# Performance work log

Hardware: AMD Instinct MI355X
Metric: run time of the kernel (lower is better)

## Reference

```python
import jax, jax.numpy as jnp
import numpy as np
from jax import lax

N, T, H, E = 50000, 200, 128, 1600000


def setup_inputs() -> dict:
    key = jax.random.key(0)
    ks = jax.random.split(key, 32)
    s = 0.05
    inp = {}
    inp["lightcurve"] = jax.random.normal(ks[0], (N, T), dtype=jnp.float32)
    inp["edge_index"] = jax.random.randint(ks[1], (2, E), 0, N, dtype=jnp.int32)
    # LSTM layer 0 (input_dim=1) and layer 1 (input H), PyTorch gate order i,f,g,o
    inp["W_ih0"] = jax.random.normal(ks[2], (4 * H, 1), jnp.float32) * s
    inp["W_hh0"] = jax.random.normal(ks[3], (4 * H, H), jnp.float32) * s
    inp["b_ih0"] = jnp.zeros((4 * H,), jnp.float32)
    inp["b_hh0"] = jnp.zeros((4 * H,), jnp.float32)
    inp["W_ih1"] = jax.random.normal(ks[4], (4 * H, H), jnp.float32) * s
    inp["W_hh1"] = jax.random.normal(ks[5], (4 * H, H), jnp.float32) * s
    inp["b_ih1"] = jnp.zeros((4 * H,), jnp.float32)
    inp["b_hh1"] = jnp.zeros((4 * H,), jnp.float32)
    # 3 GCN conv layers + LayerNorms
    for i in range(3):
        inp[f"Wg{i}"] = jax.random.normal(ks[6 + i], (H, H), jnp.float32) * s
        inp[f"bg{i}"] = jnp.zeros((H,), jnp.float32)
        inp[f"gamma{i}"] = jnp.ones((H,), jnp.float32)
        inp[f"beta{i}"] = jnp.zeros((H,), jnp.float32)
    inp["W_out"] = jax.random.normal(ks[10], (H, 1), jnp.float32) * s
    inp["b_out"] = jnp.zeros((1,), jnp.float32)
    return inp


def _lstm_encode(x, W_ih0, W_hh0, b_ih0, b_hh0, W_ih1, W_hh1, b_ih1, b_hh1):
    # x: [N, T, 1] -> final hidden of layer 2: [N, H]. Both layers fused in one scan.
    n = x.shape[0]
    h = W_hh0.shape[1]

    def cell(xt, hs, cs, Wih, Whh, bih, bhh):
        g = xt @ Wih.T + hs @ Whh.T + (bih + bhh)
        i, f, gg, o = jnp.split(g, 4, axis=-1)
        cs = jax.nn.sigmoid(f) * cs + jax.nn.sigmoid(i) * jnp.tanh(gg)
        hs = jax.nn.sigmoid(o) * jnp.tanh(cs)
        return hs, cs

    def step(carry, x_t):
        h1, c1, h2, c2 = carry
        h1, c1 = cell(x_t, h1, c1, W_ih0, W_hh0, b_ih0, b_hh0)
        h2, c2 = cell(h1, h2, c2, W_ih1, W_hh1, b_ih1, b_hh1)
        return (h1, c1, h2, c2), None

    z = jnp.zeros((n, h), x.dtype)
    (_, _, h2, _), _ = lax.scan(step, (z, z, z, z), jnp.swapaxes(x, 0, 1))
    return h2


def _forward(lightcurve, W_ih0, W_hh0, b_ih0, b_hh0, W_ih1, W_hh1, b_ih1, b_hh1,
             Wg0, bg0, gamma0, beta0, Wg1, bg1, gamma1, beta1, Wg2, bg2, gamma2, beta2,
             W_out, b_out, edge_index):
    n = lightcurve.shape[0]
    h = _lstm_encode(lightcurve[..., None], W_ih0, W_hh0, b_ih0, b_hh0,
                     W_ih1, W_hh1, b_ih1, b_hh1)
    # GCN normalization (PyG GCNConv defaults: add self-loops, symmetric norm)
    loops = jnp.arange(n, dtype=edge_index.dtype)
    row = jnp.concatenate([edge_index[0], loops])  # source
    col = jnp.concatenate([edge_index[1], loops])  # target
    deg = jax.ops.segment_sum(jnp.ones_like(col, dtype=h.dtype), col, num_segments=n)
    dinv = lax.rsqrt(jnp.maximum(deg, 1.0))
    enorm = dinv[row] * dinv[col]  # [E+N]
    for Wg, bg, gm, bt in ((Wg0, bg0, gamma0, beta0), (Wg1, bg1, gamma1, beta1), (Wg2, bg2, gamma2, beta2)):
        h_prev = h
        msg = (h @ Wg)[row] * enorm[:, None]            # gather + scale
        h = jax.ops.segment_sum(msg, col, num_segments=n) + bg  # scatter-add
        mu = h.mean(-1, keepdims=True)                  # LayerNorm
        var = jnp.mean((h - mu) ** 2, axis=-1, keepdims=True)
        h = (h - mu) * lax.rsqrt(var + 1e-5) * gm + bt
        h = jax.nn.relu(h)
        h = h + h_prev  # dropout is identity in eval mode
    pooled = h.mean(axis=0, keepdims=True)  # [1, H]
    return pooled @ W_out + b_out           # [1, 1]


def reference(lightcurve, edge_index, W_ih0, W_hh0, b_ih0, b_hh0,
              W_ih1, W_hh1, b_ih1, b_hh1,
              Wg0, bg0, gamma0, beta0, Wg1, bg1, gamma1, beta1,
              Wg2, bg2, gamma2, beta2, W_out, b_out):
    return _forward(lightcurve, W_ih0, W_hh0, b_ih0, b_hh0, W_ih1, W_hh1, b_ih1, b_hh1,
                    Wg0, bg0, gamma0, beta0, Wg1, bg1, gamma1, beta1,
                    Wg2, bg2, gamma2, beta2, W_out, b_out, edge_index)
```

## Files before the change

### kernel.cpp

```cpp
#include <hip/hip_runtime.h>

#define NN 50000
#define TT 200
#define HH 128
#define EE 1600000

#define NL2E  -1.4426950408889634f
#define TWOL2E 2.8853900817779268f

typedef _Float16 f16x8 __attribute__((ext_vector_type(8)));
typedef float f32x4 __attribute__((ext_vector_type(4)));

__device__ __forceinline__ float sg2(float x) {
    return __builtin_amdgcn_rcpf(1.f + __builtin_amdgcn_exp2f(x));
}
__device__ __forceinline__ float th2(float x) {
    return 1.f - 2.f * __builtin_amdgcn_rcpf(__builtin_amdgcn_exp2f(x) + 1.f);
}
__device__ __forceinline__ f32x4 sg2_4(f32x4 x) {
    f32x4 r; r[0] = sg2(x[0]); r[1] = sg2(x[1]); r[2] = sg2(x[2]); r[3] = sg2(x[3]); return r;
}
__device__ __forceinline__ f32x4 th2_4(f32x4 x) {
    f32x4 r; r[0] = th2(x[0]); r[1] = th2(x[1]); r[2] = th2(x[2]); r[3] = th2(x[3]); return r;
}
__device__ __forceinline__ f32x4 splat4(float s) { f32x4 r = {s, s, s, s}; return r; }
__device__ __forceinline__ unsigned short f2h_bits(float x) {
    _Float16 h = (_Float16)x;
    union { _Float16 h; unsigned short u; } cv; cv.h = h; return cv.u;
}
__device__ __forceinline__ float h2f_bits(unsigned short u) {
    union { _Float16 h; unsigned short u; } cv; cv.u = u; return (float)cv.h;
}

__global__ void pack_w(const float* __restrict__ W, unsigned short* __restrict__ out) {
    int tile = blockIdx.x;
    int jn = tile >> 2, kk = tile & 3;
    int L = threadIdx.x;
    int n = jn * 16 + (L & 15);
    int k0 = kk * 32 + (L >> 4) * 8;
    float sc = ((jn >> 3) == 2) ? TWOL2E : NL2E;
    unsigned short* dst = out + (size_t)tile * 512 + L * 8;
#pragma unroll
    for (int i = 0; i < 8; ++i) dst[i] = f2h_bits(W[n * 128 + k0 + i] * sc);
}

__global__ void bias_prep(const float* __restrict__ bih0, const float* __restrict__ bhh0,
                          const float* __restrict__ bih1, const float* __restrict__ bhh1,
                          const float* __restrict__ wih0,
                          float* __restrict__ b0g, float* __restrict__ b1g, float* __restrict__ wxg) {
    int i = blockIdx.x * 256 + threadIdx.x;
    if (i < 512) {
        float sc = ((i >> 7) == 2) ? TWOL2E : NL2E;
        b0g[i] = (bih0[i] + bhh0[i]) * sc;
        b1g[i] = (bih1[i] + bhh1[i]) * sc;
        wxg[i] = wih0[i] * sc;
    }
}

__global__ void transpose_lc(const float* __restrict__ lc, float* __restrict__ xT) {
    __shared__ float tile[32][33];
    int tx = threadIdx.x, ty = threadIdx.y;
    int n0 = blockIdx.y * 32, t0 = blockIdx.x * 32;
#pragma unroll
    for (int i = 0; i < 32; i += 8) {
        int n = n0 + ty + i, t = t0 + tx;
        if (n < NN && t < TT) tile[ty + i][tx] = lc[(size_t)n * TT + t];
    }
    __syncthreads();
#pragma unroll
    for (int i = 0; i < 32; i += 8) {
        int t = t0 + ty + i, n = n0 + tx;
        if (n < NN && t < TT) xT[(size_t)t * NN + n] = tile[tx][ty + i];
    }
}


#define MFMA16(A, B, C) __builtin_amdgcn_mfma_f32_16x16x32_f16((A), (B), (C), 0, 0, 0)

#define MMC(HB, PI, PF, PG, PO, KK) {                                          \
    f16x8 bI_ = *reinterpret_cast<const f16x8*>((PI) + (KK) * 512);            \
    f16x8 bF_ = *reinterpret_cast<const f16x8*>((PF) + (KK) * 512);            \
    f16x8 bG_ = *reinterpret_cast<const f16x8*>((PG) + (KK) * 512);            \
    f16x8 bO_ = *reinterpret_cast<const f16x8*>((PO) + (KK) * 512);            \
    f16x8 a0_ = *reinterpret_cast<const f16x8*>(&(HB)[col][(KK) * 32 + quad * 8]);      \
    f16x8 a1_ = *reinterpret_cast<const f16x8*>(&(HB)[16 + col][(KK) * 32 + quad * 8]); \
    aI0 = MFMA16(a0_, bI_, aI0); aI1 = MFMA16(a1_, bI_, aI1);                  \
    aF0 = MFMA16(a0_, bF_, aF0); aF1 = MFMA16(a1_, bF_, aF1);                  \
    aG0 = MFMA16(a0_, bG_, aG0); aG1 = MFMA16(a1_, bG_, aG1);                  \
    aO0 = MFMA16(a0_, bO_, aO0); aO1 = MFMA16(a1_, bO_, aO1);                  \
}

#define ACT0N(RT, C, H, AI, AF, AG, AO) {                                      \
    f32x4 xv_ = *reinterpret_cast<const f32x4*>(&xs[(RT) * 16 + quad * 4]);    \
    f32x4 gi_ = AI + splat4(bI) + xv_ * splat4(wI);                            \
    f32x4 gf_ = AF + splat4(bF) + xv_ * splat4(wF);                            \
    f32x4 gg_ = AG + splat4(bG) + xv_ * splat4(wG);                            \
    f32x4 go_ = AO + splat4(bO) + xv_ * splat4(wO);                            \
    C = sg2_4(gf_) * C + sg2_4(gi_) * th2_4(gg_);                              \
    H = sg2_4(go_) * th2_4(C * splat4(TWOL2E));                                \
}

#define ACT1N(C, H, AI, AF, AG, AO) {                                          \
    f32x4 gi_ = AI + splat4(bI);                                               \
    f32x4 gf_ = AF + splat4(bF);                                               \
    f32x4 gg_ = AG + splat4(bG);                                               \
    f32x4 go_ = AO + splat4(bO);                                               \
    C = sg2_4(gf_) * C + sg2_4(gi_) * th2_4(gg_);                              \
    H = sg2_4(go_) * th2_4(C * splat4(TWOL2E));                                \
}

#define WRH(HB, RT, H)                                                         \
    (HB)[(RT) * 16 + quad * 4 + 0][j_] = f2h_bits((H)[0]);                     \
    (HB)[(RT) * 16 + quad * 4 + 1][j_] = f2h_bits((H)[1]);                     \
    (HB)[(RT) * 16 + quad * 4 + 2][j_] = f2h_bits((H)[2]);                     \
    (HB)[(RT) * 16 + quad * 4 + 3][j_] = f2h_bits((H)[3]);

#define STEP(PB, RB, T)                                                        \
    {                      \
        f32x4 aI0 = {}, aI1 = {}, aF0 = {}, aF1 = {};                          \
        f32x4 aG0 = {}, aG1 = {}, aO0 = {}, aO1 = {};                          \
        MMC(h1s[RB], p0I, p0F, p0G, p0O, 0)                                    \
        MMC(h1s[RB], p0I, p0F, p0G, p0O, 1)                                    \
        MMC(h1s[RB], p0I, p0F, p0G, p0O, 2)                                    \
        MMC(h1s[RB], p0I, p0F, p0G, p0O, 3)                                    \
        const float bI = b0s[j_], bF = b0s[128 + j_];                          \
        const float bG = b0s[256 + j_], bO = b0s[384 + j_];                    \
        const float wI = wxs[j_], wF = wxs[128 + j_];                          \
        const float wG = wxs[256 + j_], wO = wxs[384 + j_];                    \
        f32x4 h1v0, h1v1;                                                      \
        ACT0N(0, c1_0, h1v0, aI0, aF0, aG0, aO0)                               \
        ACT0N(1, c1_1, h1v1, aI1, aF1, aG1, aO1)                               \
        WRH(h1s[PB], 0, h1v0)                                                  \
        WRH(h1s[PB], 1, h1v1)                                                  \
    }                                                                          \
    __syncthreads();                                                           \
    {             \
        f32x4 aI0 = {}, aI1 = {}, aF0 = {}, aF1 = {};                          \
        f32x4 aG0 = {}, aG1 = {}, aO0 = {}, aO1 = {};                          \
        MMC(h1s[PB], u0I, u0F, u0G, u0O, 0)                                    \
        MMC(h1s[PB], u0I, u0F, u0G, u0O, 1)                                    \
        MMC(h1s[PB], u0I, u0F, u0G, u0O, 2)                                    \
        MMC(h1s[PB], u0I, u0F, u0G, u0O, 3)                                    \
        MMC(h2s[RB], v0I, v0F, v0G, v0O, 0)                                    \
        MMC(h2s[RB], v0I, v0F, v0G, v0O, 1)                                    \
        MMC(h2s[RB], v0I, v0F, v0G, v0O, 2)                                    \
        MMC(h2s[RB], v0I, v0F, v0G, v0O, 3)                                    \
        if (tid < 32) {                    \
            int n_ = n0 + tid;                                                 \
            xs[tid] = ((T) + 1 < TT && n_ < NN)                                \
                          ? xT[(size_t)((T) + 1) * NN + n_] : 0.f;             \
        }                                                                      \
        const float bI = b1s[j_], bF = b1s[128 + j_];                          \
        const float bG = b1s[256 + j_], bO = b1s[384 + j_];                    \
        f32x4 h2v0, h2v1;                                                      \
        ACT1N(c2_0, h2v0, aI0, aF0, aG0, aO0)                                  \
        ACT1N(c2_1, h2v1, aI1, aF1, aG1, aO1)                                  \
        WRH(h2s[PB], 0, h2v0)                                                  \
        WRH(h2s[PB], 1, h2v1)                                                  \
    }                                                                          \
    __syncthreads();

__global__ __launch_bounds__(512, 2) void lstm_kernel(
    const float* __restrict__ xT,
    const unsigned short* __restrict__ w0p,
    const unsigned short* __restrict__ w1ip,
    const unsigned short* __restrict__ w1hp,
    const float* __restrict__ b0g, const float* __restrict__ b1g,
    const float* __restrict__ wxg,
    float* __restrict__ h2out) {
    __shared__ unsigned short h1s[2][32][136];
    __shared__ unsigned short h2s[2][32][136];
    __shared__ __align__(16) float xs[32];
    __shared__ float b0s[512], b1s[512], wxs[512];

    const int tid = threadIdx.x;
    const int w = tid >> 6;
    const int lane = tid & 63;
    const int col = lane & 15;
    const int quad = lane >> 4;
    const int n0 = blockIdx.x * 32;
    const int j_ = w * 16 + col;

    for (int i = tid; i < 2 * 32 * 136; i += 512) {
        (&h1s[0][0][0])[i] = 0; (&h2s[0][0][0])[i] = 0;
    }
    if (tid < 512) { b0s[tid] = b0g[tid]; b1s[tid] = b1g[tid]; wxs[tid] = wxg[tid]; }
    if (tid < 32) { int n = n0 + tid; xs[tid] = (n < NN) ? xT[n] : 0.f; }

    const unsigned short* p0I = w0p + (size_t)w * 2048 + lane * 8;
    const unsigned short* p0F = w0p + (size_t)(8 + w) * 2048 + lane * 8;
    const unsigned short* p0G = w0p + (size_t)(16 + w) * 2048 + lane * 8;
    const unsigned short* p0O = w0p + (size_t)(24 + w) * 2048 + lane * 8;
    const unsigned short* u0I = w1ip + (size_t)w * 2048 + lane * 8;
    const unsigned short* u0F = w1ip + (size_t)(8 + w) * 2048 + lane * 8;
    const unsigned short* u0G = w1ip + (size_t)(16 + w) * 2048 + lane * 8;
    const unsigned short* u0O = w1ip + (size_t)(24 + w) * 2048 + lane * 8;
    const unsigned short* v0I = w1hp + (size_t)w * 2048 + lane * 8;
    const unsigned short* v0F = w1hp + (size_t)(8 + w) * 2048 + lane * 8;
    const unsigned short* v0G = w1hp + (size_t)(16 + w) * 2048 + lane * 8;
    const unsigned short* v0O = w1hp + (size_t)(24 + w) * 2048 + lane * 8;

    f32x4 c1_0 = {}, c1_1 = {}, c2_0 = {}, c2_1 = {};

    __syncthreads();

#pragma unroll 1
    for (int tt = 0; tt < TT; tt += 2) {
        STEP(0, 1, tt)
        STEP(1, 0, tt + 1)
    }

    for (int i = tid; i < 32 * 128; i += 512) {
        int m = i >> 7, j = i & 127;
        int n = n0 + m;
        if (n < NN) h2out[(size_t)n * HH + j] = h2f_bits(h2s[1][m][j]);
    }
}

__global__ void deg_init(float* __restrict__ deg) {
    int i = blockIdx.x * 256 + threadIdx.x;
    if (i < NN) deg[i] = 1.f;
}
__global__ void deg_edges(const int* __restrict__ ei, float* __restrict__ deg) {
    int e = blockIdx.x * 256 + threadIdx.x;
    if (e < EE) unsafeAtomicAdd(&deg[ei[EE + e]], 1.f);
}
__global__ void dinv_k(const float* __restrict__ deg, float* __restrict__ dinv) {
    int i = blockIdx.x * 256 + threadIdx.x;
    if (i < NN) dinv[i] = rsqrtf(fmaxf(deg[i], 1.f));
}

__global__ void scan_off(const float* __restrict__ deg, int* __restrict__ off) {
    __shared__ int sp[256];
    const int tid = threadIdx.x;
    const int chunk = (NN + 255) / 256;
    const int i0 = tid * chunk;
    int s = 0;
    for (int i = 0; i < chunk; ++i) {
        int idx = i0 + i;
        if (idx < NN) s += (int)deg[idx] - 1;
    }
    sp[tid] = s;
    __syncthreads();
    for (int o = 1; o < 256; o <<= 1) {
        int v = (tid >= o) ? sp[tid - o] : 0;
        __syncthreads();
        sp[tid] += v;
        __syncthreads();
    }
    int run = sp[tid] - s;
    for (int i = 0; i < chunk; ++i) {
        int idx = i0 + i;
        if (idx < NN) { off[idx] = run; run += (int)deg[idx] - 1; }
    }
    if (tid == 255) off[NN] = sp[255];
}

__global__ void csr_fill(const int* __restrict__ ei, const float* __restrict__ dinv,
                         const int* __restrict__ off, int* __restrict__ cur,
                         int* __restrict__ crow, float* __restrict__ cw) {
    int e = blockIdx.x * 256 + threadIdx.x;
    if (e >= EE) return;
    int r = ei[e], c = ei[EE + e];
    int p = atomicAdd(&cur[c], 1);
    int idx = off[c] + p;
    crow[idx] = r;
    cw[idx] = dinv[r] * dinv[c];
}

__global__ void gcn_gemm(const float* __restrict__ h, const float* __restrict__ Wg,
                         float* __restrict__ hw) {
    __shared__ float hsT[128][36];
    int tid = threadIdx.x;
    int n0 = blockIdx.x * 32;
#pragma unroll
    for (int c = 0; c < 16; ++c) {
        int lin = c * 256 + tid;
        int m = lin >> 7, k = lin & 127;
        int n = n0 + m;
        hsT[k][m] = (n < NN) ? h[(size_t)n * HH + k] : 0.f;
    }
    __syncthreads();
    int j = tid & 127, p = tid >> 7;
    float acc[16];
#pragma unroll
    for (int m = 0; m < 16; ++m) acc[m] = 0.f;
    for (int k = 0; k < 128; ++k) {
        float wg = Wg[k * 128 + j];
        const float4* hp = reinterpret_cast<const float4*>(&hsT[k][p * 16]);
        float4 a = hp[0], b = hp[1], c = hp[2], d = hp[3];
        acc[0]  += a.x * wg; acc[1]  += a.y * wg; acc[2]  += a.z * wg; acc[3]  += a.w * wg;
        acc[4]  += b.x * wg; acc[5]  += b.y * wg; acc[6]  += b.z * wg; acc[7]  += b.w * wg;
        acc[8]  += c.x * wg; acc[9]  += c.y * wg; acc[10] += c.z * wg; acc[11] += c.w * wg;
        acc[12] += d.x * wg; acc[13] += d.y * wg; acc[14] += d.z * wg; acc[15] += d.w * wg;
    }
#pragma unroll
    for (int m = 0; m < 16; ++m) {
        int n = n0 + p * 16 + m;
        if (n < NN) hw[(size_t)n * HH + j] = acc[m];
    }
}

__global__ __launch_bounds__(256) void gcn_agg(
    const float* __restrict__ hw, const int* __restrict__ off,
    const int* __restrict__ crow, const float* __restrict__ cw,
    const float* __restrict__ dinv, const float* __restrict__ bg,
    const float* __restrict__ gamma, const float* __restrict__ beta,
    float* __restrict__ h) {
    __shared__ float xch[4][2];
    const int tid = threadIdx.x;
    const int half = tid >> 7;
    const int f = tid & 127;
    const int v = blockIdx.x * 2 + half;
    const float d = dinv[v];
    float acc = bg[f] + d * d * hw[v * HH + f];
    const int s1 = off[v + 1];
    for (int s = off[v]; s < s1; ++s) {
        int r = crow[s];
        float wv = cw[s];
        acc = fmaf(wv, hw[r * HH + f], acc);
    }
    float sum = acc, sq = acc * acc;
#pragma unroll
    for (int o = 32; o; o >>= 1) { sum += __shfl_xor(sum, o); sq += __shfl_xor(sq, o); }
    int wid = tid >> 6;
    if ((tid & 63) == 0) { xch[wid][0] = sum; xch[wid][1] = sq; }
    __syncthreads();
    sum += xch[wid ^ 1][0]; sq += xch[wid ^ 1][1];
    float mu = sum * (1.f / 128.f);
    float var = sq * (1.f / 128.f) - mu * mu;
    float rn = rsqrtf(var + 1e-5f);
    float o = (acc - mu) * rn * gamma[f] + beta[f];
    h[v * HH + f] = fmaxf(o, 0.f) + h[v * HH + f];
}

__global__ void pool_k(const float* __restrict__ h, float* __restrict__ pooled) {
    int j = threadIdx.x & 127, p = threadIdx.x >> 7;
    float s = 0.f;
    for (int n = blockIdx.x * 2 + p; n < NN; n += 512) s += h[(size_t)n * HH + j];
    unsafeAtomicAdd(&pooled[j], s);
}

__global__ void final_k(const float* __restrict__ pooled, const float* __restrict__ Wout,
                        const float* __restrict__ bout, float* __restrict__ out) {
    int lane = threadIdx.x;
    float s = pooled[lane] * Wout[lane] + pooled[lane + 64] * Wout[lane + 64];
#pragma unroll
    for (int o = 32; o; o >>= 1) s += __shfl_xor(s, o);
    if (lane == 0) out[0] = s * (1.f / (float)NN) + bout[0];
}

extern "C" void kernel_launch(void* const* d_in, const int* in_sizes, int n_in,
                              void* d_out, int out_size, void* d_ws, size_t ws_size,
                              hipStream_t stream) {
    const float* lc   = (const float*)d_in[0];
    const int*   ei   = (const int*)d_in[1];
    const float* Wih0 = (const float*)d_in[2];
    const float* Whh0 = (const float*)d_in[3];
    const float* bih0 = (const float*)d_in[4];
    const float* bhh0 = (const float*)d_in[5];
    const float* Wih1 = (const float*)d_in[6];
    const float* Whh1 = (const float*)d_in[7];
    const float* bih1 = (const float*)d_in[8];
    const float* bhh1 = (const float*)d_in[9];
    const float* Wout = (const float*)d_in[22];
    const float* bout = (const float*)d_in[23];
    float* out = (float*)d_out;

    float* ws   = (float*)d_ws;
    float* h    = ws;
    float* hw   = ws + 6400000;
    float* xT   = ws + 6400000;
    int*   off  = (int*)(ws + 12800000);
    int*   cur  = off + 50048;
    int*   crow = cur + 50048;
    float* cw   = (float*)(crow + EE);
    float* P      = ws + 16400064;
    float* deg    = P;
    float* dinv   = deg + 50000;
    float* b0g    = dinv + 50000;
    float* b1g    = b0g + 512;
    float* wxg    = b1g + 512;
    float* pooled = wxg + 512;
    unsigned short* w0p  = (unsigned short*)(pooled + 128);
    unsigned short* w1ip = w0p + 65536;
    unsigned short* w1hp = w1ip + 65536;

    pack_w<<<128, 64, 0, stream>>>(Whh0, w0p);
    pack_w<<<128, 64, 0, stream>>>(Wih1, w1ip);
    pack_w<<<128, 64, 0, stream>>>(Whh1, w1hp);
    bias_prep<<<2, 256, 0, stream>>>(bih0, bhh0, bih1, bhh1, Wih0, b0g, b1g, wxg);
    {
        dim3 g((TT + 31) / 32, (NN + 31) / 32), b(32, 8);
        transpose_lc<<<g, b, 0, stream>>>(lc, xT);
    }
    deg_init<<<(NN + 255) / 256, 256, 0, stream>>>(deg);
    deg_edges<<<(EE + 255) / 256, 256, 0, stream>>>(ei, deg);
    dinv_k<<<(NN + 255) / 256, 256, 0, stream>>>(deg, dinv);

    lstm_kernel<<<(NN + 31) / 32, 512, 0, stream>>>(xT, w0p, w1ip, w1hp, b0g, b1g, wxg, h);

    hipMemsetAsync(cur, 0, 50000 * sizeof(int), stream);
    scan_off<<<1, 256, 0, stream>>>(deg, off);
    csr_fill<<<(EE + 255) / 256, 256, 0, stream>>>(ei, dinv, off, cur, crow, cw);

    for (int l = 0; l < 3; ++l) {
        const float* Wg = (const float*)d_in[10 + 4 * l];
        const float* bg = (const float*)d_in[11 + 4 * l];
        const float* gm = (const float*)d_in[12 + 4 * l];
        const float* bt = (const float*)d_in[13 + 4 * l];
        gcn_gemm<<<(NN + 31) / 32, 256, 0, stream>>>(h, Wg, hw);
        gcn_agg<<<NN / 2, 256, 0, stream>>>(hw, off, crow, cw, dinv, bg, gm, bt, h);
    }

    hipMemsetAsync(pooled, 0, HH * sizeof(float), stream);
    pool_k<<<256, 256, 0, stream>>>(h, pooled);
    final_k<<<1, 64, 0, stream>>>(pooled, Wout, bout, out);
}
```

Before: 7.786 ms.

## Halve LSTM block to 256 threads with each wave covering two hidden column groups

The LSTM kernel now launches 4 waves per block instead of 8. Each wave handles two 16-column hidden slices (j and j+64), so per-wave MFMA work doubles and the cell/hidden state registers double. Weight offsets become 32-bit indices into the packed matrices rather than twelve precomputed pointers. The aim is to cut the cost of block-wide barriers across fewer waves and to gain more instruction-level parallelism per wave. In exchange, register pressure rises and there are fewer waves available to hide latency.

Result: slower. 17.74 ms (+127.8%).

```diff
diff --git a/kernel.cpp b/kernel.cpp
--- a/kernel.cpp
+++ b/kernel.cpp
@@ -77,11 +77,14 @@
 
 #define MFMA16(A, B, C) __builtin_amdgcn_mfma_f32_16x16x32_f16((A), (B), (C), 0, 0, 0)
 
-#define MMC(HB, PI, PF, PG, PO, KK) {                                          \
-    f16x8 bI_ = *reinterpret_cast<const f16x8*>((PI) + (KK) * 512);            \
-    f16x8 bF_ = *reinterpret_cast<const f16x8*>((PF) + (KK) * 512);            \
-    f16x8 bG_ = *reinterpret_cast<const f16x8*>((PG) + (KK) * 512);            \
-    f16x8 bO_ = *reinterpret_cast<const f16x8*>((PO) + (KK) * 512);            \
+#define LD8(MAT, VO, KK) \
+    (*reinterpret_cast<const f16x8*>(&(MAT)[(size_t)(VO) + (KK) * 512]))
+
+#define MMCG(HB, MAT, VI, VF, VG, VOO, KK) {                                   \
+    f16x8 bI_ = LD8(MAT, VI, KK);                                              \
+    f16x8 bF_ = LD8(MAT, VF, KK);                                              \
+    f16x8 bG_ = LD8(MAT, VG, KK);                                              \
+    f16x8 bO_ = LD8(MAT, VOO, KK);                                             \
     f16x8 a0_ = *reinterpret_cast<const f16x8*>(&(HB)[col][(KK) * 32 + quad * 8]);      \
     f16x8 a1_ = *reinterpret_cast<const f16x8*>(&(HB)[16 + col][(KK) * 32 + quad * 8]); \
     aI0 = MFMA16(a0_, bI_, aI0); aI1 = MFMA16(a1_, bI_, aI1);                  \
@@ -109,58 +112,64 @@
     H = sg2_4(go_) * th2_4(C * splat4(TWOL2E));                                \
 }
 
-#define WRH(HB, RT, H)                                                         \
-    (HB)[(RT) * 16 + quad * 4 + 0][j_] = f2h_bits((H)[0]);                     \
-    (HB)[(RT) * 16 + quad * 4 + 1][j_] = f2h_bits((H)[1]);                     \
-    (HB)[(RT) * 16 + quad * 4 + 2][j_] = f2h_bits((H)[2]);                     \
-    (HB)[(RT) * 16 + quad * 4 + 3][j_] = f2h_bits((H)[3]);
+#define WRH(HB, RT, H, J)                                                      \
+    (HB)[(RT) * 16 + quad * 4 + 0][J] = f2h_bits((H)[0]);                      \
+    (HB)[(RT) * 16 + quad * 4 + 1][J] = f2h_bits((H)[1]);                      \
+    (HB)[(RT) * 16 + quad * 4 + 2][J] = f2h_bits((H)[2]);                      \
+    (HB)[(RT) * 16 + quad * 4 + 3][J] = f2h_bits((H)[3]);
+
+#define L0_GROUP(RB, PB, J, VI, VF, VG, VO_, C0, C1) {                         \
+    f32x4 aI0 = {}, aI1 = {}, aF0 = {}, aF1 = {};                              \
+    f32x4 aG0 = {}, aG1 = {}, aO0 = {}, aO1 = {};                              \
+    MMCG(h1s[RB], w0p, VI, VF, VG, VO_, 0)                                     \
+    MMCG(h1s[RB], w0p, VI, VF, VG, VO_, 1)                                     \
+    MMCG(h1s[RB], w0p, VI, VF, VG, VO_, 2)                                     \
+    MMCG(h1s[RB], w0p, VI, VF, VG, VO_, 3)                                     \
+    const float bI = b0s[J], bF = b0s[128 + (J)];                              \
+    const float bG = b0s[256 + (J)], bO = b0s[384 + (J)];                      \
+    const float wI = wxs[J], wF = wxs[128 + (J)];                              \
+    const float wG = wxs[256 + (J)], wO = wxs[384 + (J)];                      \
+    f32x4 h1v0, h1v1;                                                          \
+    ACT0N(0, C0, h1v0, aI0, aF0, aG0, aO0)                                     \
+    ACT0N(1, C1, h1v1, aI1, aF1, aG1, aO1)                                     \
+    WRH(h1s[PB], 0, h1v0, J)                                                   \
+    WRH(h1s[PB], 1, h1v1, J)                                                   \
+}
+
+#define L1_GROUP(RB, PB, J, VI, VF, VG, VO_, C0, C1) {                         \
+    f32x4 aI0 = {}, aI1 = {}, aF0 = {}, aF1 = {};                              \
+    f32x4 aG0 = {}, aG1 = {}, aO0 = {}, aO1 = {};                              \
+    MMCG(h1s[PB], w1ip, VI, VF, VG, VO_, 0)                                    \
+    MMCG(h1s[PB], w1ip, VI, VF, VG, VO_, 1)                                    \
+    MMCG(h1s[PB], w1ip, VI, VF, VG, VO_, 2)                                    \
+    MMCG(h1s[PB], w1ip, VI, VF, VG, VO_, 3)                                    \
+    MMCG(h2s[RB], w1hp, VI, VF, VG, VO_, 0)                                    \
+    MMCG(h2s[RB], w1hp, VI, VF, VG, VO_, 1)                                    \
+    MMCG(h2s[RB], w1hp, VI, VF, VG, VO_, 2)                                    \
+    MMCG(h2s[RB], w1hp, VI, VF, VG, VO_, 3)                                    \
+    const float bI = b1s[J], bF = b1s[128 + (J)];                              \
+    const float bG = b1s[256 + (J)], bO = b1s[384 + (J)];                      \
+    f32x4 h2v0, h2v1;                                                          \
+    ACT1N(C0, h2v0, aI0, aF0, aG0, aO0)                                        \
+    ACT1N(C1, h2v1, aI1, aF1, aG1, aO1)                                        \
+    WRH(h2s[PB], 0, h2v0, J)                                                   \
+    WRH(h2s[PB], 1, h2v1, J)                                                   \
+}
 
 #define STEP(PB, RB, T)                                                        \
-    {                      \
-        f32x4 aI0 = {}, aI1 = {}, aF0 = {}, aF1 = {};                          \
-        f32x4 aG0 = {}, aG1 = {}, aO0 = {}, aO1 = {};                          \
-        MMC(h1s[RB], p0I, p0F, p0G, p0O, 0)                                    \
-        MMC(h1s[RB], p0I, p0F, p0G, p0O, 1)                                    \
-        MMC(h1s[RB], p0I, p0F, p0G, p0O, 2)                                    \
-        MMC(h1s[RB], p0I, p0F, p0G, p0O, 3)                                    \
-        const float bI = b0s[j_], bF = b0s[128 + j_];                          \
-        const float bG = b0s[256 + j_], bO = b0s[384 + j_];                    \
-        const float wI = wxs[j_], wF = wxs[128 + j_];                          \
-        const float wG = wxs[256 + j_], wO = wxs[384 + j_];                    \
-        f32x4 h1v0, h1v1;                                                      \
-        ACT0N(0, c1_0, h1v0, aI0, aF0, aG0, aO0)                               \
-        ACT0N(1, c1_1, h1v1, aI1, aF1, aG1, aO1)                               \
-        WRH(h1s[PB], 0, h1v0)                                                  \
-        WRH(h1s[PB], 1, h1v1)                                                  \
+    L0_GROUP(RB, PB, jA, vAI, vAF, vAG, vAO, c1A0, c1A1)                       \
+    L0_GROUP(RB, PB, jB, vBI, vBF, vBG, vBO, c1B0, c1B1)                       \
+    __syncthreads();                                                           \
+    L1_GROUP(RB, PB, jA, vAI, vAF, vAG, vAO, c2A0, c2A1)                       \
+    if (tid < 32) {           \
+        int n_ = n0 + tid;                                                     \
+        xs[tid] = ((T) + 1 < TT && n_ < NN)                                    \
+                      ? xT[(size_t)((T) + 1) * NN + n_] : 0.f;                 \
     }                                                                          \
-    __syncthreads();                                                           \
-    {             \
-        f32x4 aI0 = {}, aI1 = {}, aF0 = {}, aF1 = {};                          \
-        f32x4 aG0 = {}, aG1 = {}, aO0 = {}, aO1 = {};                          \
-        MMC(h1s[PB], u0I, u0F, u0G, u0O, 0)                                    \
-        MMC(h1s[PB], u0I, u0F, u0G, u0O, 1)                                    \
-        MMC(h1s[PB], u0I, u0F, u0G, u0O, 2)                                    \
-        MMC(h1s[PB], u0I, u0F, u0G, u0O, 3)                                    \
-        MMC(h2s[RB], v0I, v0F, v0G, v0O, 0)                                    \
-        MMC(h2s[RB], v0I, v0F, v0G, v0O, 1)                                    \
-        MMC(h2s[RB], v0I, v0F, v0G, v0O, 2)                                    \
-        MMC(h2s[RB], v0I, v0F, v0G, v0O, 3)                                    \
-        if (tid < 32) {                    \
-            int n_ = n0 + tid;                                                 \
-            xs[tid] = ((T) + 1 < TT && n_ < NN)                                \
-                          ? xT[(size_t)((T) + 1) * NN + n_] : 0.f;             \
-        }                                                                      \
-        const float bI = b1s[j_], bF = b1s[128 + j_];                          \
-        const float bG = b1s[256 + j_], bO = b1s[384 + j_];                    \
-        f32x4 h2v0, h2v1;                                                      \
-        ACT1N(c2_0, h2v0, aI0, aF0, aG0, aO0)                                  \
-        ACT1N(c2_1, h2v1, aI1, aF1, aG1, aO1)                                  \
-        WRH(h2s[PB], 0, h2v0)                                                  \
-        WRH(h2s[PB], 1, h2v1)                                                  \
-    }                                                                          \
-    __syncthreads();
-
-__global__ __launch_bounds__(512, 2) void lstm_kernel(
+    L1_GROUP(RB, PB, jB, vBI, vBF, vBG, vBO, c2B0, c2B1)                       \
+    __syncthreads();
+
+__global__ __launch_bounds__(256, 2) void lstm_kernel(
     const float* __restrict__ xT,
     const unsigned short* __restrict__ w0p,
     const unsigned short* __restrict__ w1ip,
@@ -174,33 +183,33 @@
     __shared__ float b0s[512], b1s[512], wxs[512];
 
     const int tid = threadIdx.x;
-    const int w = tid >> 6;
+    const int w4 = tid >> 6;
     const int lane = tid & 63;
     const int col = lane & 15;
     const int quad = lane >> 4;
     const int n0 = blockIdx.x * 32;
-    const int j_ = w * 16 + col;
-
-    for (int i = tid; i < 2 * 32 * 136; i += 512) {
+    const int jA = w4 * 16 + col;
+    const int jB = jA + 64;
+
+    for (int i = tid; i < 2 * 32 * 136; i += 256) {
         (&h1s[0][0][0])[i] = 0; (&h2s[0][0][0])[i] = 0;
     }
-    if (tid < 512) { b0s[tid] = b0g[tid]; b1s[tid] = b1g[tid]; wxs[tid] = wxg[tid]; }
+    for (int i = tid; i < 512; i += 256) {
+        b0s[i] = b0g[i]; b1s[i] = b1g[i]; wxs[i] = wxg[i];
+    }
     if (tid < 32) { int n = n0 + tid; xs[tid] = (n < NN) ? xT[n] : 0.f; }
 
-    const unsigned short* p0I = w0p + (size_t)w * 2048 + lane * 8;
-    const unsigned short* p0F = w0p + (size_t)(8 + w) * 2048 + lane * 8;
-    const unsigned short* p0G = w0p + (size_t)(16 + w) * 2048 + lane * 8;
-    const unsigned short* p0O = w0p + (size_t)(24 + w) * 2048 + lane * 8;
-    const unsigned short* u0I = w1ip + (size_t)w * 2048 + lane * 8;
-    const unsigned short* u0F = w1ip + (size_t)(8 + w) * 2048 + lane * 8;
-    const unsigned short* u0G = w1ip + (size_t)(16 + w) * 2048 + lane * 8;
-    const unsigned short* u0O = w1ip + (size_t)(24 + w) * 2048 + lane * 8;
-    const unsigned short* v0I = w1hp + (size_t)w * 2048 + lane * 8;
-    const unsigned short* v0F = w1hp + (size_t)(8 + w) * 2048 + lane * 8;
-    const unsigned short* v0G = w1hp + (size_t)(16 + w) * 2048 + lane * 8;
-    const unsigned short* v0O = w1hp + (size_t)(24 + w) * 2048 + lane * 8;
-
-    f32x4 c1_0 = {}, c1_1 = {}, c2_0 = {}, c2_1 = {};
+    const unsigned int vAI = (unsigned int)((0 * 8 + w4) * 2048 + lane * 8);
+    const unsigned int vAF = vAI + 8 * 2048;
+    const unsigned int vAG = vAI + 16 * 2048;
+    const unsigned int vAO = vAI + 24 * 2048;
+    const unsigned int vBI = vAI + 4 * 2048;
+    const unsigned int vBF = vBI + 8 * 2048;
+    const unsigned int vBG = vBI + 16 * 2048;
+    const unsigned int vBO = vBI + 24 * 2048;
+
+    f32x4 c1A0 = {}, c1A1 = {}, c1B0 = {}, c1B1 = {};
+    f32x4 c2A0 = {}, c2A1 = {}, c2B0 = {}, c2B1 = {};
 
     __syncthreads();
 
@@ -210,7 +219,7 @@
         STEP(1, 0, tt + 1)
     }
 
-    for (int i = tid; i < 32 * 128; i += 512) {
+    for (int i = tid; i < 32 * 128; i += 256) {
         int m = i >> 7, j = i & 127;
         int n = n0 + m;
         if (n < NN) h2out[(size_t)n * HH + j] = h2f_bits(h2s[1][m][j]);
@@ -398,7 +407,7 @@
     deg_edges<<<(EE + 255) / 256, 256, 0, stream>>>(ei, deg);
     dinv_k<<<(NN + 255) / 256, 256, 0, stream>>>(deg, dinv);
 
-    lstm_kernel<<<(NN + 31) / 32, 512, 0, stream>>>(xT, w0p, w1ip, w1hp, b0g, b1g, wxg, h);
+    lstm_kernel<<<(NN + 31) / 32, 256, 0, stream>>>(xT, w0p, w1ip, w1hp, b0g, b1g, wxg, h);
 
     hipMemsetAsync(cur, 0, 50000 * sizeof(int), stream);
     scan_off<<<1, 256, 0, stream>>>(deg, off);
```
